# Performance work log

Hardware: AMD Instinct MI355X
Metric: run time of the kernel (lower is better)

The kernel has to match this reference:

```python
import jax, jax.numpy as jnp
import numpy as np

B, S, H, V = 256, 15, 512, 50257

def setup_inputs() -> dict:
    key = jax.random.key(0)
    ks = jax.random.split(key, 12)
    sc_h = 1.0 / np.sqrt(H)
    sc_in = 1.0 / np.sqrt(2 * H)
    return {
        "input_tokens": jax.random.randint(ks[0], (B, 1), 0, V),
        "hidden": jax.random.normal(ks[1], (1, B, H), jnp.float32),
        "encoder_outputs": jax.random.normal(ks[2], (B, S, H), jnp.float32),
        "emb_table": jax.random.normal(ks[3], (V, H), jnp.float32),
        "attn_W": jax.random.uniform(ks[4], (H, H), jnp.float32, -sc_h, sc_h),
        "attn_b": jax.random.uniform(ks[5], (H,), jnp.float32, -sc_h, sc_h),
        "W_ih": jax.random.uniform(ks[6], (3 * H, 2 * H), jnp.float32, -sc_in, sc_in),
        "W_hh": jax.random.uniform(ks[7], (3 * H, H), jnp.float32, -sc_h, sc_h),
        "b_ih": jax.random.uniform(ks[8], (3 * H,), jnp.float32, -sc_h, sc_h),
        "b_hh": jax.random.uniform(ks[9], (3 * H,), jnp.float32, -sc_h, sc_h),
        "out_W": jax.random.uniform(ks[10], (V, H), jnp.float32, -sc_h, sc_h),
        "out_b": jax.random.uniform(ks[11], (V,), jnp.float32, -sc_h, sc_h),
    }


def reference(input_tokens, hidden, encoder_outputs, emb_table, attn_W, attn_b,
              W_ih, W_hh, b_ih, b_hh, out_W, out_b):
    # Embedding (dropout is identity in eval/reference mode): [B,1,H]
    embedded = emb_table[input_tokens]
    h = hidden[0]  # [B,H]

    # Bahdanau-style scores, vectorized over the seq dim instead of the python loop:
    # energies[b,s] = attn(enc[b,s]);  score[b,s] = <h[b], energies[b,s]>
    energies = jnp.einsum("bsh,oh->bso", encoder_outputs, attn_W) + attn_b  # [B,S,H]
    attn_scores = jnp.einsum("bso,bo->bs", energies, h)                      # [B,S]
    attn_weights = jax.nn.softmax(attn_scores, axis=1)                       # [B,S]

    # context = weights @ encoder_outputs: [B,1,H]
    context = jnp.einsum("bs,bsh->bh", attn_weights, encoder_outputs)[:, None, :]

    # GRU single step (PyTorch gate order: r, z, n)
    x = jnp.concatenate([embedded, context], axis=2)[:, 0]  # [B,2H]
    gi = x @ W_ih.T + b_ih   # [B,3H]
    gh = h @ W_hh.T + b_hh   # [B,3H]
    i_r, i_z, i_n = jnp.split(gi, 3, axis=1)
    h_r, h_z, h_n = jnp.split(gh, 3, axis=1)
    r = jax.nn.sigmoid(i_r + h_r)
    z = jax.nn.sigmoid(i_z + h_z)
    n = jnp.tanh(i_n + r * h_n)
    h_new = (1.0 - z) * n + z * h            # [B,H]

    logits = h_new[:, None, :] @ out_W.T + out_b   # [B,1,V]
    log_probs = jax.nn.log_softmax(logits, axis=-1)
    return log_probs, h_new[None], attn_weights
```

## Files before the change

kernel.cpp:

```cpp
#include <hip/hip_runtime.h>

#define V_SIZE 50257
#define B_SIZE 256
#define S_LEN  15
#define H_DIM  512
#define NBLK_LG 786

typedef __attribute__((ext_vector_type(8))) short bf16x8;
typedef __attribute__((ext_vector_type(4))) float f32x4;

__device__ __forceinline__ unsigned short f2bf(float f) {
    unsigned int u = __float_as_uint(f);
    u += 0x7fffu + ((u >> 16) & 1u);
    return (unsigned short)(u >> 16);
}

__global__ __launch_bounds__(256) void u_kernel(
    const float* __restrict__ hidden, const float* __restrict__ attn_W,
    float* __restrict__ u)
{
    __shared__ float h_s[16][H_DIM];
    const int tid = threadIdx.x;
    const int b0 = blockIdx.y * 16, n0 = blockIdx.x * 32;
    const float4* hv = (const float4*)(hidden + (size_t)b0 * H_DIM);
    float4* hs4 = (float4*)&h_s[0][0];
    #pragma unroll
    for (int i = 0; i < 8; ++i) hs4[tid + i * 256] = hv[tid + i * 256];
    __syncthreads();
    const int n = n0 + (tid & 31);
    const int m = (tid >> 5) * 2;
    float a0 = 0.f, a1 = 0.f;
    #pragma unroll 8
    for (int o = 0; o < H_DIM; ++o) {
        float w = attn_W[(size_t)o * H_DIM + n];
        a0 += h_s[m][o] * w;
        a1 += h_s[m + 1][o] * w;
    }
    u[(size_t)(b0 + m) * H_DIM + n] = a0;
    u[(size_t)(b0 + m + 1) * H_DIM + n] = a1;
}

__global__ __launch_bounds__(256) void attn_kernel(
    const float* __restrict__ hidden, const float* __restrict__ enc,
    const float* __restrict__ u, const int* __restrict__ tokens,
    const float* __restrict__ emb, float* __restrict__ attnw_out,
    unsigned short* __restrict__ x_bf, unsigned short* __restrict__ h_bf)
{
    const int b = blockIdx.x, tid = threadIdx.x;
    __shared__ float u_s[H_DIM];
    __shared__ float sc_s[S_LEN];
    __shared__ float w_s[S_LEN];
    u_s[tid]       = u[(size_t)b * H_DIM + tid];
    u_s[tid + 256] = u[(size_t)b * H_DIM + tid + 256];
    h_bf[(size_t)b * H_DIM + tid]       = f2bf(hidden[(size_t)b * H_DIM + tid]);
    h_bf[(size_t)b * H_DIM + tid + 256] = f2bf(hidden[(size_t)b * H_DIM + tid + 256]);
    const int tok = tokens[b];
    x_bf[(size_t)b * 2 * H_DIM + tid]       = f2bf(emb[(size_t)tok * H_DIM + tid]);
    x_bf[(size_t)b * 2 * H_DIM + tid + 256] = f2bf(emb[(size_t)tok * H_DIM + tid + 256]);
    __syncthreads();
    const int wave = tid >> 6, lane = tid & 63;
    for (int s = wave; s < S_LEN; s += 4) {
        const float* e = enc + ((size_t)b * S_LEN + s) * H_DIM;
        float acc = 0.f;
        #pragma unroll
        for (int k = 0; k < H_DIM / 64; ++k) acc += e[lane + k * 64] * u_s[lane + k * 64];
        #pragma unroll
        for (int off = 32; off; off >>= 1) acc += __shfl_down(acc, off);
        if (lane == 0) sc_s[s] = acc;
    }
    __syncthreads();
    float mx = -1e30f;
    for (int s = 0; s < S_LEN; ++s) mx = fmaxf(mx, sc_s[s]);
    float sum = 0.f;
    for (int s = 0; s < S_LEN; ++s) sum += __expf(sc_s[s] - mx);
    const float inv = 1.f / sum;
    if (tid < S_LEN) {
        float w = __expf(sc_s[tid] - mx) * inv;
        w_s[tid] = w;
        attnw_out[b * S_LEN + tid] = w;
    }
    __syncthreads();
    #pragma unroll
    for (int hh = 0; hh < 2; ++hh) {
        int h = tid + hh * 256;
        float c = 0.f;
        #pragma unroll
        for (int s = 0; s < S_LEN; ++s)
            c += w_s[s] * enc[((size_t)b * S_LEN + s) * H_DIM + h];
        x_bf[(size_t)b * 2 * H_DIM + H_DIM + h] = f2bf(c);
    }
}

struct GemmP {
    const unsigned short* A; const float* B; const float* bias; float* C;
    int N; int K;
};

template<int BM, int BN, int BK, int WR, int WC>
__global__ __launch_bounds__(256) void gemm_nt(GemmP p0, GemmP p1)
{
    GemmP p = (blockIdx.z == 0) ? p0 : p1;
    constexpr int LDA = BK + 8;
    __shared__ __align__(16) unsigned short As[BM][LDA];
    __shared__ __align__(16) unsigned short Bs[BN][LDA];
    const int tid = threadIdx.x;
    const int bn0 = blockIdx.x * BN;
    const int bm0 = blockIdx.y * BM;
    const int wave = tid >> 6, lane = tid & 63;
    const int wm = (wave / WC) * (BM / WR);
    const int wn = (wave % WC) * (BN / WC);
    constexpr int MF = BM / WR / 16, NF = BN / WC / 16;
    const int n16 = lane & 15, quad = lane >> 4;

    f32x4 acc[MF][NF] = {};

    for (int k0 = 0; k0 < p.K; k0 += BK) {
        #pragma unroll
        for (int it = 0; it < BM / 32; ++it) {
            int v = it * 256 + tid;
            int row = v >> 3, seg = v & 7;
            *(uint4*)&As[row][seg * 8] =
                *(const uint4*)(p.A + (size_t)(bm0 + row) * p.K + k0 + seg * 8);
        }
        #pragma unroll
        for (int it = 0; it < BN / 32; ++it) {
            int v = it * 256 + tid;
            int row = v >> 3, seg = v & 7;
            int gv = bn0 + row;
            float4 w0 = make_float4(0, 0, 0, 0), w1 = make_float4(0, 0, 0, 0);
            if (gv < p.N) {
                const float4* src = (const float4*)(p.B + (size_t)gv * p.K + k0 + seg * 8);
                w0 = src[0]; w1 = src[1];
            }
            uint4 pk;
            pk.x = (unsigned)f2bf(w0.x) | ((unsigned)f2bf(w0.y) << 16);
            pk.y = (unsigned)f2bf(w0.z) | ((unsigned)f2bf(w0.w) << 16);
            pk.z = (unsigned)f2bf(w1.x) | ((unsigned)f2bf(w1.y) << 16);
            pk.w = (unsigned)f2bf(w1.z) | ((unsigned)f2bf(w1.w) << 16);
            *(uint4*)&Bs[row][seg * 8] = pk;
        }
        __syncthreads();
        #pragma unroll
        for (int kk = 0; kk < BK; kk += 32) {
            bf16x8 af[MF], bfr[NF];
            #pragma unroll
            for (int i = 0; i < MF; ++i)
                af[i] = *(const bf16x8*)&As[wm + i * 16 + n16][kk + quad * 8];
            #pragma unroll
            for (int j = 0; j < NF; ++j)
                bfr[j] = *(const bf16x8*)&Bs[wn + j * 16 + n16][kk + quad * 8];
            #pragma unroll
            for (int i = 0; i < MF; ++i)
                #pragma unroll
                for (int j = 0; j < NF; ++j)
                    acc[i][j] = __builtin_amdgcn_mfma_f32_16x16x32_bf16(
                        af[i], bfr[j], acc[i][j], 0, 0, 0);
        }
        __syncthreads();
    }
    #pragma unroll
    for (int i = 0; i < MF; ++i) {
        const int r0 = bm0 + wm + i * 16 + quad * 4;
        #pragma unroll
        for (int j = 0; j < NF; ++j) {
            const int c = bn0 + wn + j * 16 + n16;
            if (c < p.N) {
                const float bv = p.bias[c];
                #pragma unroll
                for (int r = 0; r < 4; ++r)
                    p.C[(size_t)(r0 + r) * p.N + c] = acc[i][j][r] + bv;
            }
        }
    }
}

template<bool PART>
__global__ __launch_bounds__(256, 4) void gemm_lg(
    const unsigned short* __restrict__ A, const float* __restrict__ B,
    const float* __restrict__ bias, float* __restrict__ C,
    float* __restrict__ pm, float* __restrict__ ps)
{
    constexpr int BN = 64, BK = 128;
    constexpr int LDB = BK + 8;
    __shared__ __align__(16) unsigned short Bs[BN][LDB];
    const int tid = threadIdx.x;
    const int bn0 = blockIdx.x * BN;
    const int wave = tid >> 6, lane = tid & 63;
    const int wm = wave * 64;
    const int n16 = lane & 15, quad = lane >> 4;

    f32x4 acc[4][4] = {};
    const unsigned short* arow[4];
    #pragma unroll
    for (int i = 0; i < 4; ++i) arow[i] = A + (size_t)(wm + i * 16 + n16) * H_DIM;

    for (int k0 = 0; k0 < H_DIM; k0 += BK) {
        #pragma unroll
        for (int it = 0; it < 4; ++it) {
            int v = it * 256 + tid;
            int row = v >> 4, seg = v & 15;
            int gv = bn0 + row;
            float4 w0 = make_float4(0, 0, 0, 0), w1 = make_float4(0, 0, 0, 0);
            if (gv < V_SIZE) {
                const float4* src = (const float4*)(B + (size_t)gv * H_DIM + k0 + seg * 8);
                w0 = src[0]; w1 = src[1];
            }
            uint4 pk;
            pk.x = (unsigned)f2bf(w0.x) | ((unsigned)f2bf(w0.y) << 16);
            pk.y = (unsigned)f2bf(w0.z) | ((unsigned)f2bf(w0.w) << 16);
            pk.z = (unsigned)f2bf(w1.x) | ((unsigned)f2bf(w1.y) << 16);
            pk.w = (unsigned)f2bf(w1.z) | ((unsigned)f2bf(w1.w) << 16);
            *(uint4*)&Bs[row][seg * 8] = pk;
        }
        __syncthreads();
        #pragma unroll
        for (int kk = 0; kk < BK; kk += 32) {
            bf16x8 af[4], bfr[4];
            #pragma unroll
            for (int i = 0; i < 4; ++i)
                af[i] = *(const bf16x8*)(arow[i] + k0 + kk + quad * 8);
            #pragma unroll
            for (int j = 0; j < 4; ++j)
                bfr[j] = *(const bf16x8*)&Bs[j * 16 + n16][kk + quad * 8];
            #pragma unroll
            for (int i = 0; i < 4; ++i)
                #pragma unroll
                for (int j = 0; j < 4; ++j)
                    acc[i][j] = __builtin_amdgcn_mfma_f32_16x16x32_bf16(
                        af[i], bfr[j], acc[i][j], 0, 0, 0);
        }
        __syncthreads();
    }

    int cj[4]; float bvv[4]; bool okj[4];
    #pragma unroll
    for (int j = 0; j < 4; ++j) {
        cj[j] = bn0 + j * 16 + n16;
        okj[j] = cj[j] < V_SIZE;
        bvv[j] = okj[j] ? bias[cj[j]] : 0.f;
    }
    #pragma unroll
    for (int i = 0; i < 4; ++i) {
        const int r0 = wm + i * 16 + quad * 4;
        if (PART) {
            #pragma unroll
            for (int r = 0; r < 4; ++r) {
                float m = -1e30f;
                #pragma unroll
                for (int j = 0; j < 4; ++j)
                    if (okj[j]) m = fmaxf(m, acc[i][j][r] + bvv[j]);
                #pragma unroll
                for (int d = 1; d < 16; d <<= 1) m = fmaxf(m, __shfl_xor(m, d));
                float s = 0.f;
                #pragma unroll
                for (int j = 0; j < 4; ++j)
                    if (okj[j]) s += __expf(acc[i][j][r] + bvv[j] - m);
                #pragma unroll
                for (int d = 1; d < 16; d <<= 1) s += __shfl_xor(s, d);
                if (n16 == 0) {
                    pm[(size_t)blockIdx.x * B_SIZE + r0 + r] = m;
                    ps[(size_t)blockIdx.x * B_SIZE + r0 + r] = s;
                }
            }
        }
        #pragma unroll
        for (int j = 0; j < 4; ++j) if (okj[j]) {
            #pragma unroll
            for (int r = 0; r < 4; ++r)
                C[(size_t)(r0 + r) * V_SIZE + cj[j]] = acc[i][j][r] + bvv[j];
        }
    }
}

__global__ __launch_bounds__(256) void gru_kernel(
    const float* __restrict__ gi, const float* __restrict__ gh,
    const float* __restrict__ hidden, float* __restrict__ hnew_out,
    unsigned short* __restrict__ hnew_bf)
{
    const int idx = blockIdx.x * 256 + threadIdx.x;
    const int b = idx >> 9, h = idx & 511;
    const float* gib = gi + (size_t)b * 3 * H_DIM;
    const float* ghb = gh + (size_t)b * 3 * H_DIM;
    float r = 1.f / (1.f + __expf(-(gib[h] + ghb[h])));
    float z = 1.f / (1.f + __expf(-(gib[H_DIM + h] + ghb[H_DIM + h])));
    float n = gib[2 * H_DIM + h] + r * ghb[2 * H_DIM + h];
    n = 1.f - 2.f / (1.f + __expf(2.f * n));
    float hp = hidden[idx];
    float hn = (1.f - z) * n + z * hp;
    hnew_out[idx] = hn;
    hnew_bf[idx] = f2bf(hn);
}

__global__ __launch_bounds__(1024) void finalize_kernel(
    float* __restrict__ logits, const float* __restrict__ pm,
    const float* __restrict__ ps)
{
    const int b = blockIdx.x, tid = threadIdx.x;
    float m = -1e30f, s = 0.f;
    for (int i = tid; i < NBLK_LG; i += 1024) {
        float mm = pm[(size_t)i * B_SIZE + b], ss = ps[(size_t)i * B_SIZE + b];
        float nm = fmaxf(m, mm);
        s = s * __expf(m - nm) + ss * __expf(mm - nm);
        m = nm;
    }
    const int lane = tid & 63, wave = tid >> 6;
    #pragma unroll
    for (int off = 32; off; off >>= 1) {
        float m2 = __shfl_down(m, off), s2 = __shfl_down(s, off);
        float nm = fmaxf(m, m2);
        s = s * __expf(m - nm) + s2 * __expf(m2 - nm);
        m = nm;
    }
    __shared__ float msh[16], ssh[16], lse_sh;
    if (lane == 0) { msh[wave] = m; ssh[wave] = s; }
    __syncthreads();
    if (tid == 0) {
        float M = msh[0], S = ssh[0];
        for (int w = 1; w < 16; ++w) {
            float nm = fmaxf(M, msh[w]);
            S = S * __expf(M - nm) + ssh[w] * __expf(msh[w] - nm);
            M = nm;
        }
        lse_sh = M + logf(S);
    }
    __syncthreads();
    const float lse = lse_sh;
    constexpr int HALF = (V_SIZE + 1) / 2;
    const int start = blockIdx.y * HALF;
    const int end = min(V_SIZE, start + HALF);
    float* row = logits + (size_t)b * V_SIZE;
    for (int c = start + tid; c < end; c += 1024) row[c] -= lse;
}

__global__ __launch_bounds__(1024) void logsoftmax_kernel(float* __restrict__ logits)
{
    const int b = blockIdx.x, tid = threadIdx.x;
    float* row = logits + (size_t)b * V_SIZE;
    float m = -1e30f, s = 0.f;
    for (int c = tid; c < V_SIZE; c += 1024) {
        float x = row[c];
        float nm = fmaxf(m, x);
        s = s * __expf(m - nm) + __expf(x - nm);
        m = nm;
    }
    const int lane = tid & 63, wave = tid >> 6;
    #pragma unroll
    for (int off = 32; off; off >>= 1) {
        float m2 = __shfl_down(m, off), s2 = __shfl_down(s, off);
        float nm = fmaxf(m, m2);
        s = s * __expf(m - nm) + s2 * __expf(m2 - nm);
        m = nm;
    }
    __shared__ float msh[16], ssh[16], lse_sh;
    if (lane == 0) { msh[wave] = m; ssh[wave] = s; }
    __syncthreads();
    if (tid == 0) {
        float M = msh[0], S = ssh[0];
        for (int w = 1; w < 16; ++w) {
            float nm = fmaxf(M, msh[w]);
            S = S * __expf(M - nm) + ssh[w] * __expf(msh[w] - nm);
            M = nm;
        }
        lse_sh = M + logf(S);
    }
    __syncthreads();
    const float lse = lse_sh;
    for (int c = tid; c < V_SIZE; c += 1024) row[c] -= lse;
}

constexpr size_t OFF_U      = 0;
constexpr size_t OFF_XBF    = 524288;
constexpr size_t OFF_HBF    = 1048576;
constexpr size_t OFF_HNEWBF = 1310720;
constexpr size_t OFF_GI     = 1572864;
constexpr size_t OFF_GH     = 3145728;
constexpr size_t OFF_PM     = 4718592;
constexpr size_t OFF_PS     = 5523456;
constexpr size_t WS_NEED    = 6328320;

extern "C" void kernel_launch(void* const* d_in, const int* in_sizes, int n_in,
                              void* d_out, int out_size, void* d_ws, size_t ws_size,
                              hipStream_t stream) {
    const int*   tokens = (const int*)d_in[0];
    const float* hidden = (const float*)d_in[1];
    const float* enc    = (const float*)d_in[2];
    const float* emb    = (const float*)d_in[3];
    const float* attn_W = (const float*)d_in[4];
    const float* W_ih   = (const float*)d_in[6];
    const float* W_hh   = (const float*)d_in[7];
    const float* b_ih   = (const float*)d_in[8];
    const float* b_hh   = (const float*)d_in[9];
    const float* out_W  = (const float*)d_in[10];
    const float* out_b  = (const float*)d_in[11];

    float* out = (float*)d_out;
    float* logp      = out;
    float* hnew_out  = out + (size_t)B_SIZE * V_SIZE;
    float* attnw_out = hnew_out + (size_t)B_SIZE * H_DIM;

    char* ws = (char*)d_ws;
    float*          u_ws    = (float*)(ws + OFF_U);
    unsigned short* x_bf    = (unsigned short*)(ws + OFF_XBF);
    unsigned short* h_bf    = (unsigned short*)(ws + OFF_HBF);
    unsigned short* hnew_bf = (unsigned short*)(ws + OFF_HNEWBF);
    float*          gi_ws   = (float*)(ws + OFF_GI);
    float*          gh_ws   = (float*)(ws + OFF_GH);
    float*          pm_ws   = (float*)(ws + OFF_PM);
    float*          ps_ws   = (float*)(ws + OFF_PS);

    u_kernel<<<dim3(16, 16), 256, 0, stream>>>(hidden, attn_W, u_ws);
    attn_kernel<<<dim3(256), 256, 0, stream>>>(hidden, enc, u_ws, tokens, emb,
                                               attnw_out, x_bf, h_bf);
    GemmP gi_p { x_bf, W_ih, b_ih, gi_ws, 3 * H_DIM, 2 * H_DIM };
    GemmP gh_p { h_bf, W_hh, b_hh, gh_ws, 3 * H_DIM, H_DIM };
    gemm_nt<64, 64, 64, 2, 2><<<dim3(24, 4, 2), 256, 0, stream>>>(gi_p, gh_p);
    gru_kernel<<<dim3(512), 256, 0, stream>>>(gi_ws, gh_ws, hidden, hnew_out, hnew_bf);

    if (ws_size >= WS_NEED) {
        gemm_lg<true><<<dim3(NBLK_LG), 256, 0, stream>>>(
            hnew_bf, out_W, out_b, logp, pm_ws, ps_ws);
        finalize_kernel<<<dim3(256, 2), 1024, 0, stream>>>(logp, pm_ws, ps_ws);
    } else {
        gemm_lg<false><<<dim3(NBLK_LG), 256, 0, stream>>>(
            hnew_bf, out_W, out_b, logp, nullptr, nullptr);
        logsoftmax_kernel<<<dim3(256), 1024, 0, stream>>>(logp);
    }
}
```

Measured before the change: 369.7 us.

## Stage encoder rows in LDS, load full-K B tile with swizzle, vectorize lse subtraction

The attention kernel now copies each batch's 15x512 encoder block into shared memory once, so the score dot products and the context sum both read it from there instead of reading global memory twice. The logits GEMM loads the entire K=512 bf16 B tile into an XOR-swizzled shared buffer in one pass, which removes the per-K-chunk barriers and bank conflicts; the larger LDS footprint lowers the occupancy hint from 4 to 2 blocks per CU. The final log-softmax subtraction pass now uses float4 accesses, with scalar head and tail handling for misalignment. Lower occupancy may reduce latency hiding in the memory-bound GEMM.

```diff
diff --git a/kernel.cpp b/kernel.cpp
--- a/kernel.cpp
+++ b/kernel.cpp
@@ -47,9 +47,19 @@
     unsigned short* __restrict__ x_bf, unsigned short* __restrict__ h_bf)
 {
     const int b = blockIdx.x, tid = threadIdx.x;
+    __shared__ float e_s[S_LEN][H_DIM];
     __shared__ float u_s[H_DIM];
     __shared__ float sc_s[S_LEN];
     __shared__ float w_s[S_LEN];
+    {
+        const float4* ev = (const float4*)(enc + (size_t)b * S_LEN * H_DIM);
+        float4* es4 = (float4*)&e_s[0][0];
+        #pragma unroll
+        for (int i = 0; i < 8; ++i) {
+            int idx = i * 256 + tid;
+            if (idx < S_LEN * H_DIM / 4) es4[idx] = ev[idx];
+        }
+    }
     u_s[tid]       = u[(size_t)b * H_DIM + tid];
     u_s[tid + 256] = u[(size_t)b * H_DIM + tid + 256];
     h_bf[(size_t)b * H_DIM + tid]       = f2bf(hidden[(size_t)b * H_DIM + tid]);
@@ -60,10 +70,10 @@
     __syncthreads();
     const int wave = tid >> 6, lane = tid & 63;
     for (int s = wave; s < S_LEN; s += 4) {
-        const float* e = enc + ((size_t)b * S_LEN + s) * H_DIM;
         float acc = 0.f;
         #pragma unroll
-        for (int k = 0; k < H_DIM / 64; ++k) acc += e[lane + k * 64] * u_s[lane + k * 64];
+        for (int k = 0; k < H_DIM / 64; ++k)
+            acc += e_s[s][lane + k * 64] * u_s[lane + k * 64];
         #pragma unroll
         for (int off = 32; off; off >>= 1) acc += __shfl_down(acc, off);
         if (lane == 0) sc_s[s] = acc;
@@ -86,7 +96,7 @@
         float c = 0.f;
         #pragma unroll
         for (int s = 0; s < S_LEN; ++s)
-            c += w_s[s] * enc[((size_t)b * S_LEN + s) * H_DIM + h];
+            c += w_s[s] * e_s[s][h];
         x_bf[(size_t)b * 2 * H_DIM + H_DIM + h] = f2bf(c);
     }
 }
@@ -175,61 +185,60 @@
 }
 
 template<bool PART>
-__global__ __launch_bounds__(256, 4) void gemm_lg(
+__global__ __launch_bounds__(256, 2) void gemm_lg(
     const unsigned short* __restrict__ A, const float* __restrict__ B,
     const float* __restrict__ bias, float* __restrict__ C,
     float* __restrict__ pm, float* __restrict__ ps)
 {
-    constexpr int BN = 64, BK = 128;
-    constexpr int LDB = BK + 8;
-    __shared__ __align__(16) unsigned short Bs[BN][LDB];
+    constexpr int BN = 64;
+    __shared__ __align__(16) unsigned short Bs[BN][H_DIM];
     const int tid = threadIdx.x;
     const int bn0 = blockIdx.x * BN;
     const int wave = tid >> 6, lane = tid & 63;
     const int wm = wave * 64;
     const int n16 = lane & 15, quad = lane >> 4;
+    const int sx = n16 & 7;
 
     f32x4 acc[4][4] = {};
     const unsigned short* arow[4];
     #pragma unroll
     for (int i = 0; i < 4; ++i) arow[i] = A + (size_t)(wm + i * 16 + n16) * H_DIM;
 
-    for (int k0 = 0; k0 < H_DIM; k0 += BK) {
-        #pragma unroll
-        for (int it = 0; it < 4; ++it) {
-            int v = it * 256 + tid;
-            int row = v >> 4, seg = v & 15;
-            int gv = bn0 + row;
-            float4 w0 = make_float4(0, 0, 0, 0), w1 = make_float4(0, 0, 0, 0);
-            if (gv < V_SIZE) {
-                const float4* src = (const float4*)(B + (size_t)gv * H_DIM + k0 + seg * 8);
-                w0 = src[0]; w1 = src[1];
-            }
-            uint4 pk;
-            pk.x = (unsigned)f2bf(w0.x) | ((unsigned)f2bf(w0.y) << 16);
-            pk.y = (unsigned)f2bf(w0.z) | ((unsigned)f2bf(w0.w) << 16);
-            pk.z = (unsigned)f2bf(w1.x) | ((unsigned)f2bf(w1.y) << 16);
-            pk.w = (unsigned)f2bf(w1.z) | ((unsigned)f2bf(w1.w) << 16);
-            *(uint4*)&Bs[row][seg * 8] = pk;
-        }
-        __syncthreads();
-        #pragma unroll
-        for (int kk = 0; kk < BK; kk += 32) {
-            bf16x8 af[4], bfr[4];
-            #pragma unroll
-            for (int i = 0; i < 4; ++i)
-                af[i] = *(const bf16x8*)(arow[i] + k0 + kk + quad * 8);
+    #pragma unroll
+    for (int it = 0; it < 16; ++it) {
+        int v = it * 256 + tid;
+        int row = v >> 6, seg = v & 63;
+        int gv = bn0 + row;
+        float4 w0 = make_float4(0, 0, 0, 0), w1 = make_float4(0, 0, 0, 0);
+        if (gv < V_SIZE) {
+            const float4* src = (const float4*)(B + (size_t)gv * H_DIM + seg * 8);
+            w0 = src[0]; w1 = src[1];
+        }
+        uint4 pk;
+        pk.x = (unsigned)f2bf(w0.x) | ((unsigned)f2bf(w0.y) << 16);
+        pk.y = (unsigned)f2bf(w0.z) | ((unsigned)f2bf(w0.w) << 16);
+        pk.z = (unsigned)f2bf(w1.x) | ((unsigned)f2bf(w1.y) << 16);
+        pk.w = (unsigned)f2bf(w1.z) | ((unsigned)f2bf(w1.w) << 16);
+        *(uint4*)&Bs[row][(seg ^ (row & 7)) * 8] = pk;
+    }
+    __syncthreads();
+
+    #pragma unroll 4
+    for (int kk = 0; kk < H_DIM; kk += 32) {
+        const int su = ((kk >> 3) + quad) ^ sx;
+        bf16x8 af[4], bfr[4];
+        #pragma unroll
+        for (int i = 0; i < 4; ++i)
+            af[i] = *(const bf16x8*)(arow[i] + kk + quad * 8);
+        #pragma unroll
+        for (int j = 0; j < 4; ++j)
+            bfr[j] = *(const bf16x8*)&Bs[j * 16 + n16][su * 8];
+        #pragma unroll
+        for (int i = 0; i < 4; ++i)
             #pragma unroll
             for (int j = 0; j < 4; ++j)
-                bfr[j] = *(const bf16x8*)&Bs[j * 16 + n16][kk + quad * 8];
-            #pragma unroll
-            for (int i = 0; i < 4; ++i)
-                #pragma unroll
-                for (int j = 0; j < 4; ++j)
-                    acc[i][j] = __builtin_amdgcn_mfma_f32_16x16x32_bf16(
-                        af[i], bfr[j], acc[i][j], 0, 0, 0);
-        }
-        __syncthreads();
+                acc[i][j] = __builtin_amdgcn_mfma_f32_16x16x32_bf16(
+                    af[i], bfr[j], acc[i][j], 0, 0, 0);
     }
 
     int cj[4]; float bvv[4]; bool okj[4];
@@ -325,11 +334,23 @@
     }
     __syncthreads();
     const float lse = lse_sh;
-    constexpr int HALF = (V_SIZE + 1) / 2;
+    constexpr int HALF = 25132;
     const int start = blockIdx.y * HALF;
     const int end = min(V_SIZE, start + HALF);
-    float* row = logits + (size_t)b * V_SIZE;
-    for (int c = start + tid; c < end; c += 1024) row[c] -= lse;
+    float* p0 = logits + (size_t)b * V_SIZE + start;
+    const int n = end - start;
+    const int mis = (int)(((uintptr_t)p0 >> 2) & 3);
+    int pre = mis ? (4 - mis) : 0; if (pre > n) pre = n;
+    if (tid < pre) p0[tid] -= lse;
+    const int nvec = (n - pre) >> 2;
+    float4* rv = (float4*)(p0 + pre);
+    for (int i = tid; i < nvec; i += 1024) {
+        float4 v = rv[i];
+        v.x -= lse; v.y -= lse; v.z -= lse; v.w -= lse;
+        rv[i] = v;
+    }
+    const int rem = n - pre - (nvec << 2);
+    if (tid < rem) p0[pre + (nvec << 2) + tid] -= lse;
 }
 
 __global__ __launch_bounds__(1024) void logsoftmax_kernel(float* __restrict__ logits)
```

Result: slower. 379.1 us (+2.5%).
